# Kernel tuning notes

Measured on AMD Instinct MI355X. Metric: run time of the kernel, lower is better.

## Reference

```python
import jax, jax.numpy as jnp
import numpy as np

D_MODEL = 1024
N_HEADS = 16
N_KV_HEADS = 4
HEAD_DIM = 64   # d_model // total_n_heads
KEY_DIM = 64    # defaults to head_dim
N_REP = N_HEADS // N_KV_HEADS
ATTN_SCALE = 1.0 / np.sqrt(HEAD_DIM)
B, S = 2, 2048


def apply_rope(x, cos, sin):
    # x: [B,S,H,Dh]; cos/sin: [S,Dh//2]; pairs are (x[2j], x[2j+1]) per llama-style apply_rotary_emb
    xr, xi = x[..., ::2], x[..., 1::2]
    c = cos[None, :, None, :]
    s = sin[None, :, None, :]
    out_r = xr * c - xi * s
    out_i = xr * s + xi * c
    return jnp.stack([out_r, out_i], axis=-1).reshape(x.shape)


def setup_inputs() -> dict:
    key = jax.random.key(0)
    ks = jax.random.split(key, 7)
    query = jax.random.normal(ks[0], (B, S, D_MODEL), jnp.float32)
    k_in = jax.random.normal(ks[1], (B, S, D_MODEL), jnp.float32)
    v_in = jax.random.normal(ks[2], (B, S, D_MODEL), jnp.float32)
    # real RoPE frequency tables (theta=10000)
    inv_freq = 1.0 / (10000.0 ** (np.arange(0, KEY_DIM, 2, dtype=np.float32) / KEY_DIM))
    ang = np.outer(np.arange(S, dtype=np.float32), inv_freq)  # [S, KEY_DIM//2]
    freqs_cos = jnp.asarray(np.cos(ang), jnp.float32)
    freqs_sin = jnp.asarray(np.sin(ang), jnp.float32)
    sc = D_MODEL ** -0.5
    wq = jax.random.normal(ks[3], (N_HEADS * KEY_DIM, D_MODEL), jnp.float32) * sc
    wk = jax.random.normal(ks[4], (N_KV_HEADS * KEY_DIM, D_MODEL), jnp.float32) * sc
    wv = jax.random.normal(ks[5], (N_KV_HEADS * HEAD_DIM, D_MODEL), jnp.float32) * sc
    wo = jax.random.normal(ks[6], (N_HEADS * HEAD_DIM, N_HEADS * HEAD_DIM), jnp.float32) * sc
    return {"query": query, "key": k_in, "value": v_in,
            "freqs_cos": freqs_cos, "freqs_sin": freqs_sin,
            "wq": wq, "wk": wk, "wv": wv, "wo": wo}


def reference(query, key, value, freqs_cos, freqs_sin, wq, wk, wv, wo):
    b, sq, _ = query.shape
    sk = key.shape[1]
    xq = (query @ wq.T).reshape(b, sq, N_HEADS, KEY_DIM)
    xk = (key @ wk.T).reshape(b, sk, N_KV_HEADS, KEY_DIM)
    xv = (value @ wv.T).reshape(b, sk, N_KV_HEADS, HEAD_DIM)
    xq = apply_rope(xq, freqs_cos, freqs_sin)
    xk = apply_rope(xk, freqs_cos, freqs_sin)
    # GQA: repeat kv heads (equivalent to torch repeat_kv expand+reshape)
    xk = jnp.repeat(xk, N_REP, axis=2)
    xv = jnp.repeat(xv, N_REP, axis=2)
    scores = jnp.einsum('bqhd,bkhd->bhqk', xq, xk) * ATTN_SCALE
    causal = jnp.tril(jnp.ones((sq, sk), dtype=bool))
    scores = jnp.where(causal[None, None, :, :], scores, -jnp.inf)
    attn = jax.nn.softmax(scores, axis=-1)
    out = jnp.einsum('bhqk,bkhd->bqhd', attn, xv).reshape(b, sq, N_HEADS * HEAD_DIM)
    return out @ wo.T
```

## Files before the change

### kernel.cpp

```cpp
#include <hip/hip_runtime.h>

#define DM 1024
#define NHEADS 16
#define NKVH 4
#define HDIM 64
#define NB 2
#define SEQ 2048
#define MTOK (NB*SEQ)

typedef __attribute__((ext_vector_type(4))) float f32x4;
typedef __attribute__((ext_vector_type(8))) short short8;
typedef unsigned short u16;
typedef unsigned int u32;

__device__ __forceinline__ u16 f2b(float f) {
  u32 i; __builtin_memcpy(&i, &f, 4);
  u32 r = i + 0x7fffu + ((i >> 16) & 1u);
  return (u16)(r >> 16);
}
__device__ __forceinline__ u32 cvtpk(float a, float b) {
  u32 r; asm("v_cvt_pk_bf16_f32 %0, %1, %2" : "=v"(r) : "v"(a), "v"(b)); return r;
}
__device__ __forceinline__ void gload16(const void* g, void* l) {
  __builtin_amdgcn_global_load_lds((const __attribute__((address_space(1))) u32*)g,
                                   (__attribute__((address_space(3))) u32*)l, 16, 0, 0);
}

__device__ __forceinline__ void cvt8(const float* __restrict__ src, u16* __restrict__ dst, int i) {
  float4 a = *(const float4*)(src + i);
  float4 b = *(const float4*)(src + i + 4);
  uint4 pk;
  pk.x = cvtpk(a.x, a.y);
  pk.y = cvtpk(a.z, a.w);
  pk.z = cvtpk(b.x, b.y);
  pk.w = cvtpk(b.z, b.w);
  *(uint4*)(dst + i) = pk;
}

__global__ __launch_bounds__(256) void cvt_all(const float* __restrict__ q, const float* __restrict__ k,
                                               const float* __restrict__ v, const float* __restrict__ wq,
                                               const float* __restrict__ wk, const float* __restrict__ wv,
                                               const float* __restrict__ wo, u16* oq, u16* ok, u16* ov,
                                               u16* owq, u16* owk, u16* owv, u16* owo) {
  const int ACT = (MTOK * DM) / 2048;
  const int BIG = (DM * DM) / 2048;
  const int SML = (256 * DM) / 2048;
  int bid = blockIdx.x;
  const float* s; u16* d;
  if (bid < ACT) { s = q; d = oq; }
  else if (bid < 2 * ACT) { s = k; d = ok; bid -= ACT; }
  else if (bid < 3 * ACT) { s = v; d = ov; bid -= 2 * ACT; }
  else {
    bid -= 3 * ACT;
    if (bid < BIG) { s = wq; d = owq; }
    else if (bid < 2 * BIG) { s = wo; d = owo; bid -= BIG; }
    else if (bid < 2 * BIG + SML) { s = wk; d = owk; bid -= 2 * BIG; }
    else { s = wv; d = owv; bid -= 2 * BIG + SML; }
  }
  cvt8(s, d, (bid * 256 + threadIdx.x) * 8);
}

template<int NR>
__device__ __forceinline__ void stage_tile(const u16* __restrict__ src, int k0, u16* lds,
                                           int w, int lane) {
#pragma unroll
  for (int i = 0; i < NR / 32; i++) {
    const int base = (i * 4 + w) * 1024;
    const int row = (base >> 7) + (lane >> 3);
    const int g = lane & 7;
    gload16(src + (size_t)row * DM + k0 + ((g ^ (row & 7)) << 3), (char*)lds + base);
  }
}
__device__ __forceinline__ short8 lds_frag(const u16* L, int row, int gr) {
  return *(const short8*)(L + row * 64 + ((gr ^ (row & 7)) << 3));
}

__global__ __launch_bounds__(256, 3) void gemm_qkv(const u16* __restrict__ Aq, const u16* __restrict__ Ak,
                                                   const u16* __restrict__ Av, const u16* __restrict__ wq,
                                                   const u16* __restrict__ wk, const u16* __restrict__ wv,
                                                   const float* __restrict__ cosb, const float* __restrict__ sinb,
                                                   u16* __restrict__ Qr, u16* __restrict__ Kr,
                                                   u16* __restrict__ Vt) {
  __shared__ __attribute__((aligned(16))) u16 SH[12288];
  u16* As = SH;
  u16* Bs = SH + 4096;
  const int tid = threadIdx.x, lane = tid & 63, w = tid >> 6;
  const int wr = w >> 1, wc = w & 1, lo = lane & 15, hi = lane >> 4;
  const int bx = blockIdx.x, by = blockIdx.y;
  const int m0 = bx * 64;

  const u16 *Ap, *Wp;
  int n0, mode;
  if (by < 8) { Ap = Aq; Wp = wq; n0 = by * 128; mode = 0; }
  else if (by < 10) { Ap = Ak; Wp = wk; n0 = (by - 8) * 128; mode = 1; }
  else { Ap = Av; Wp = wv; n0 = (by - 10) * 128; mode = 2; }
  const u16* Abase = Ap + (size_t)m0 * DM;
  const u16* Wbase = Wp + (size_t)n0 * DM;

  f32x4 acc[2][4];
#pragma unroll
  for (int i = 0; i < 2; i++)
#pragma unroll
    for (int j = 0; j < 4; j++) acc[i][j] = (f32x4){0.f, 0.f, 0.f, 0.f};

  for (int ks = 0; ks < 16; ks++) {
    const int k0 = ks * 64;
    stage_tile<64>(Abase, k0, As, w, lane);
    stage_tile<128>(Wbase, k0, Bs, w, lane);
    __syncthreads();
    short8 af[2][2], bfr[4][2];
#pragma unroll
    for (int mi = 0; mi < 2; mi++)
#pragma unroll
      for (int kk = 0; kk < 2; kk++)
        af[mi][kk] = lds_frag(As, wr * 32 + mi * 16 + lo, kk * 4 + hi);
#pragma unroll
    for (int ni = 0; ni < 4; ni++)
#pragma unroll
      for (int kk = 0; kk < 2; kk++)
        bfr[ni][kk] = lds_frag(Bs, wc * 64 + ni * 16 + lo, kk * 4 + hi);
    __builtin_amdgcn_s_setprio(1);
#pragma unroll
    for (int mi = 0; mi < 2; mi++)
#pragma unroll
      for (int ni = 0; ni < 4; ni++) {
        acc[mi][ni] = __builtin_amdgcn_mfma_f32_16x16x32_bf16(af[mi][0], bfr[ni][0], acc[mi][ni], 0, 0, 0);
        acc[mi][ni] = __builtin_amdgcn_mfma_f32_16x16x32_bf16(af[mi][1], bfr[ni][1], acc[mi][ni], 0, 0, 0);
      }
    __builtin_amdgcn_s_setprio(0);
    __syncthreads();
  }

  if (mode < 2) {
    const float scale = (mode == 0) ? 0.18033688f : 1.0f;
    u16* outp = (mode == 0) ? Qr : Kr;
    const int OH = (mode == 0) ? NHEADS : NKVH;
    const float sgn = (lo & 1) ? 1.0f : -1.0f;
#pragma unroll
    for (int ni = 0; ni < 4; ni++) {
      const int col = n0 + wc * 64 + ni * 16 + lo;
      const int h = col >> 6, d = col & 63, j = d >> 1;
#pragma unroll
      for (int mi = 0; mi < 2; mi++)
#pragma unroll
        for (int r = 0; r < 4; r++) {
          int row = m0 + wr * 32 + mi * 16 + hi * 4 + r;
          int srow = row & (SEQ - 1), bb = row >> 11;
          float v = acc[mi][ni][r];
          float pv = __shfl_xor(v, 1, 64);
          float c = cosb[srow * 32 + j];
          float s = sinb[srow * 32 + j];
          outp[((size_t)(bb * OH + h) * SEQ + srow) * 64 + d] = f2b((v * c + pv * s * sgn) * scale);
        }
    }
  } else {
    u16* Tt = SH;
#pragma unroll
    for (int mi = 0; mi < 2; mi++)
#pragma unroll
      for (int ni = 0; ni < 4; ni++) {
        const int cl = wc * 64 + ni * 16 + lo;
#pragma unroll
        for (int r = 0; r < 4; r++) {
          int rl = wr * 32 + mi * 16 + hi * 4 + r;
          Tt[cl * 72 + rl] = f2b(acc[mi][ni][r]);
        }
      }
    __syncthreads();
    const int dl = tid >> 1;
    const int sh2 = (tid & 1) * 32;
    const int dg = n0 + dl;
    const int kh = dg >> 6, drow = dg & 63;
    const int bb = m0 >> 11, sbase = m0 & (SEQ - 1);
    u16* dst = Vt + ((size_t)(bb * NKVH + kh) * 64 + drow) * SEQ + sbase + sh2;
#pragma unroll
    for (int i = 0; i < 4; i++)
      *(uint4*)(dst + i * 8) = *(const uint4*)&Tt[dl * 72 + sh2 + i * 8];
  }
}

__device__ __forceinline__ void softmax_pv(f32x4 (&sc)[4], float& m, float& lsp, f32x4 (&o)[4],
                                           const short8* vb0, const short8* vb1, int hi) {
  float lm = sc[0][0];
#pragma unroll
  for (int f = 0; f < 4; f++)
#pragma unroll
    for (int r = 0; r < 4; r++) lm = fmaxf(lm, sc[f][r]);
  if (__any(lm - m > 8.f)) {
    float mx = fmaxf(m, lm);
    mx = fmaxf(mx, __shfl_xor(mx, 16, 64));
    mx = fmaxf(mx, __shfl_xor(mx, 32, 64));
    float corr = exp2f(m - mx);
    m = mx;
    lsp *= corr;
    float corrq[4];
#pragma unroll
    for (int r = 0; r < 4; r++) corrq[r] = __shfl(corr, hi * 4 + r, 64);
#pragma unroll
    for (int nf = 0; nf < 4; nf++)
#pragma unroll
      for (int r = 0; r < 4; r++) o[nf][r] *= corrq[r];
  }
  float pv2[4][4];
#pragma unroll
  for (int f = 0; f < 4; f++)
#pragma unroll
    for (int r = 0; r < 4; r++) {
      pv2[f][r] = exp2f(sc[f][r] - m);
      lsp += pv2[f][r];
    }
  union { u32 u[4]; short8 s8; } pa0, pa1;
#pragma unroll
  for (int t = 0; t < 4; t++) {
    int fsel = t >> 1, r0 = 2 * (t & 1);
    pa0.u[t] = cvtpk(pv2[fsel][r0], pv2[fsel][r0 + 1]);
    pa1.u[t] = cvtpk(pv2[2 + fsel][r0], pv2[2 + fsel][r0 + 1]);
  }
  __builtin_amdgcn_s_setprio(1);
#pragma unroll
  for (int nf = 0; nf < 4; nf++) {
    o[nf] = __builtin_amdgcn_mfma_f32_16x16x32_bf16(pa0.s8, vb0[nf], o[nf], 0, 0, 0);
    o[nf] = __builtin_amdgcn_mfma_f32_16x16x32_bf16(pa1.s8, vb1[nf], o[nf], 0, 0, 0);
  }
  __builtin_amdgcn_s_setprio(0);
}

__global__ __launch_bounds__(256, 2) void attn_kernel(const u16* __restrict__ Q, const u16* __restrict__ Kb,
                                                      const u16* __restrict__ Vt, u16* __restrict__ AO) {
  __shared__ __attribute__((aligned(16))) u16 Ks[2][4096];
  __shared__ __attribute__((aligned(16))) u16 Vs[2][4096];
  const int tid = threadIdx.x;
  const int w = tid >> 6, lane = tid & 63;
  const int lo = lane & 15, hi = lane >> 4;
  const int bh = blockIdx.x;
  const int b = bh >> 4, h = bh & 15, kh = h >> 2;
  const int yy = blockIdx.y;
  const int p = (yy < 8) ? yy : 23 - yy;
  const int tA = p, tB = 31 - p;
  const int q0A = tA * 64 + w * 16;
  const int q0B = tB * 64 + w * 16;
  const u16* Qp = Q + (size_t)bh * SEQ * 64;
  const u16* Kp = Kb + (size_t)(b * NKVH + kh) * SEQ * 64;
  const u16* Vp = Vt + (size_t)(b * NKVH + kh) * 64 * SEQ;

  short8 qfA[2], qfB[2];
#pragma unroll
  for (int kk = 0; kk < 2; kk++) {
    qfA[kk] = *(const short8*)(Qp + (size_t)(q0A + lo) * 64 + kk * 32 + hi * 8);
    qfB[kk] = *(const short8*)(Qp + (size_t)(q0B + lo) * 64 + kk * 32 + hi * 8);
  }

  f32x4 oA[4], oB[4];
#pragma unroll
  for (int nf = 0; nf < 4; nf++) { oA[nf] = (f32x4){0.f,0.f,0.f,0.f}; oB[nf] = (f32x4){0.f,0.f,0.f,0.f}; }
  float mA = -__builtin_inff(), lspA = 0.f;
  float mB = -__builtin_inff(), lspB = 0.f;

  auto key = [](int row) { return (row & 3) | (((row >> 3) & 1) << 2); };
  auto stage = [&](int kv0, int bufi) {
#pragma unroll
    for (int s = 0; s < 2; s++) {
      int base = s * 4096 + w * 1024;
      int o2 = base + (lane << 4);
      int row = o2 >> 7;
      int gg = ((o2 >> 4) & 7) ^ key(row);
      gload16(Kp + (size_t)(kv0 + row) * 64 + gg * 8, (char*)&Ks[bufi][0] + base);
      gload16(Vp + (size_t)row * SEQ + kv0 + gg * 8, (char*)&Vs[bufi][0] + base);
    }
  };
  auto lds8 = [&](const u16* S, int row, int col8) {
    return *(const short8*)(S + row * 64 + (col8 ^ (key(row) << 3)));
  };

  int krow[4];
#pragma unroll
  for (int f = 0; f < 4; f++)
    krow[f] = 32 * (f >> 1) + 8 * (lo >> 2) + 4 * (f & 1) + (lo & 3);

  const int nt = tB + 1;
  stage(0, 0);
  __syncthreads();

  for (int c = 0; c < nt; ++c) {
    const int cur = c & 1;
    const int kv0 = c * 64;
    if (c + 1 < nt) stage(kv0 + 64, cur ^ 1);

    short8 kf0[4], kf1[4];
#pragma unroll
    for (int f = 0; f < 4; f++) {
      kf0[f] = lds8(&Ks[cur][0], krow[f], hi * 8);
      kf1[f] = lds8(&Ks[cur][0], krow[f], 32 + hi * 8);
    }
    const bool actA = (c <= tA);

    f32x4 scB[4], scA[4];
#pragma unroll
    for (int f = 0; f < 4; f++) scB[f] = (f32x4){0.f,0.f,0.f,0.f};
    __builtin_amdgcn_s_setprio(1);
#pragma unroll
    for (int f = 0; f < 4; f++) {
      scB[f] = __builtin_amdgcn_mfma_f32_16x16x32_bf16(kf0[f], qfB[0], scB[f], 0, 0, 0);
      scB[f] = __builtin_amdgcn_mfma_f32_16x16x32_bf16(kf1[f], qfB[1], scB[f], 0, 0, 0);
    }
    __builtin_amdgcn_s_setprio(0);
    if (actA) {
#pragma unroll
      for (int f = 0; f < 4; f++) scA[f] = (f32x4){0.f,0.f,0.f,0.f};
      __builtin_amdgcn_s_setprio(1);
#pragma unroll
      for (int f = 0; f < 4; f++) {
        scA[f] = __builtin_amdgcn_mfma_f32_16x16x32_bf16(kf0[f], qfA[0], scA[f], 0, 0, 0);
        scA[f] = __builtin_amdgcn_mfma_f32_16x16x32_bf16(kf1[f], qfA[1], scA[f], 0, 0, 0);
      }
      __builtin_amdgcn_s_setprio(0);
    }

    short8 vb0[4], vb1[4];
#pragma unroll
    for (int nf = 0; nf < 4; nf++) {
      vb0[nf] = lds8(&Vs[cur][0], nf * 16 + lo, hi * 8);
      vb1[nf] = lds8(&Vs[cur][0], nf * 16 + lo, 32 + hi * 8);
    }

    if (c == tB) {
#pragma unroll
      for (int f = 0; f < 4; f++) {
        int kvb = kv0 + 32 * (f >> 1) + 8 * hi + 4 * (f & 1);
#pragma unroll
        for (int r = 0; r < 4; r++)
          if (kvb + r > q0B + lo) scB[f][r] = -__builtin_inff();
      }
    }
    softmax_pv(scB, mB, lspB, oB, vb0, vb1, hi);

    if (actA) {
      if (c == tA) {
#pragma unroll
        for (int f = 0; f < 4; f++) {
          int kvb = kv0 + 32 * (f >> 1) + 8 * hi + 4 * (f & 1);
#pragma unroll
          for (int r = 0; r < 4; r++)
            if (kvb + r > q0A + lo) scA[f][r] = -__builtin_inff();
        }
      }
      softmax_pv(scA, mA, lspA, oA, vb0, vb1, hi);
    }
    __syncthreads();
  }

#pragma unroll
  for (int t2 = 0; t2 < 2; t2++) {
    float lsp = t2 ? lspB : lspA;
    const int q0 = t2 ? q0B : q0A;
    f32x4* o = t2 ? oB : oA;
    lsp += __shfl_xor(lsp, 16, 64);
    lsp += __shfl_xor(lsp, 32, 64);
    float inv = 1.0f / lsp;
    float invq[4];
#pragma unroll
    for (int r = 0; r < 4; r++) invq[r] = __shfl(inv, hi * 4 + r, 64);
#pragma unroll
    for (int nf = 0; nf < 4; nf++)
#pragma unroll
      for (int r = 0; r < 4; r++) {
        int q = q0 + hi * 4 + r;
        int d = nf * 16 + lo;
        AO[((size_t)(b * SEQ + q) * NHEADS + h) * 64 + d] = f2b(o[nf][r] * invq[r]);
      }
  }
}

__global__ __launch_bounds__(256, 2) void gemm_out(const u16* __restrict__ A, const u16* __restrict__ W,
                                                   float* __restrict__ Out) {
  __shared__ __attribute__((aligned(16))) u16 SH[12288];
  u16* As = SH;
  u16* Bs = SH + 4096;
  const int tid = threadIdx.x, lane = tid & 63, w = tid >> 6;
  const int wr = w >> 1, wc = w & 1, lo = lane & 15, hi = lane >> 4;
  const int m0 = blockIdx.x * 64, n0 = blockIdx.y * 128;
  const u16* Abase = A + (size_t)m0 * DM;
  const u16* Wbase = W + (size_t)n0 * DM;

  f32x4 acc[2][4];
#pragma unroll
  for (int i = 0; i < 2; i++)
#pragma unroll
    for (int j = 0; j < 4; j++) acc[i][j] = (f32x4){0.f, 0.f, 0.f, 0.f};

  for (int ks = 0; ks < 16; ks++) {
    const int k0 = ks * 64;
    stage_tile<64>(Abase, k0, As, w, lane);
    stage_tile<128>(Wbase, k0, Bs, w, lane);
    __syncthreads();
    short8 af[2][2], bfr[4][2];
#pragma unroll
    for (int mi = 0; mi < 2; mi++)
#pragma unroll
      for (int kk = 0; kk < 2; kk++)
        af[mi][kk] = lds_frag(As, wr * 32 + mi * 16 + lo, kk * 4 + hi);
#pragma unroll
    for (int ni = 0; ni < 4; ni++)
#pragma unroll
      for (int kk = 0; kk < 2; kk++)
        bfr[ni][kk] = lds_frag(Bs, wc * 64 + ni * 16 + lo, kk * 4 + hi);
    __builtin_amdgcn_s_setprio(1);
#pragma unroll
    for (int mi = 0; mi < 2; mi++)
#pragma unroll
      for (int ni = 0; ni < 4; ni++) {
        acc[mi][ni] = __builtin_amdgcn_mfma_f32_16x16x32_bf16(af[mi][0], bfr[ni][0], acc[mi][ni], 0, 0, 0);
        acc[mi][ni] = __builtin_amdgcn_mfma_f32_16x16x32_bf16(af[mi][1], bfr[ni][1], acc[mi][ni], 0, 0, 0);
      }
    __builtin_amdgcn_s_setprio(0);
    __syncthreads();
  }

#pragma unroll
  for (int mi = 0; mi < 2; mi++)
#pragma unroll
    for (int ni = 0; ni < 4; ni++)
#pragma unroll
      for (int r = 0; r < 4; r++) {
        int row = m0 + wr * 32 + mi * 16 + hi * 4 + r;
        int col = n0 + wc * 64 + ni * 16 + lo;
        Out[(size_t)row * DM + col] = acc[mi][ni][r];
      }
}

extern "C" void kernel_launch(void* const* d_in, const int* in_sizes, int n_in,
                              void* d_out, int out_size, void* d_ws, size_t ws_size,
                              hipStream_t stream) {
  const float* query = (const float*)d_in[0];
  const float* key_ = (const float*)d_in[1];
  const float* value = (const float*)d_in[2];
  const float* fcos = (const float*)d_in[3];
  const float* fsin = (const float*)d_in[4];
  const float* wq = (const float*)d_in[5];
  const float* wk = (const float*)d_in[6];
  const float* wv = (const float*)d_in[7];
  const float* wo = (const float*)d_in[8];

  char* ws = (char*)d_ws;
  size_t off = 0;
  auto alloc = [&](size_t elems) {
    u16* p = (u16*)(ws + off);
    off = (off + elems * 2 + 255) & ~(size_t)255;
    return p;
  };
  u16* qf = alloc((size_t)MTOK * DM);
  u16* kf = alloc((size_t)MTOK * DM);
  u16* vf = alloc((size_t)MTOK * DM);
  u16* wqf = alloc((size_t)DM * DM);
  u16* wkf = alloc((size_t)256 * DM);
  u16* wvf = alloc((size_t)256 * DM);
  u16* wof = alloc((size_t)DM * DM);
  u16* Qr = alloc((size_t)MTOK * DM);
  u16* Kr = alloc((size_t)NB * NKVH * SEQ * 64);
  u16* Vt = alloc((size_t)NB * NKVH * 64 * SEQ);
  u16* AO = alloc((size_t)MTOK * DM);

  cvt_all<<<3 * 2048 + 1280, 256, 0, stream>>>(query, key_, value, wq, wk, wv, wo,
                                               qf, kf, vf, wqf, wkf, wvf, wof);

  gemm_qkv<<<dim3(64, 12), 256, 0, stream>>>(qf, kf, vf, wqf, wkf, wvf,
                                             fcos, fsin, Qr, Kr, Vt);

  attn_kernel<<<dim3(NB * NHEADS, 16), 256, 0, stream>>>(Qr, Kr, Vt, AO);

  gemm_out<<<dim3(64, 8), 256, 0, stream>>>(AO, wof, (float*)d_out);
}
```

Before: 93.50 us.

## Serialize paired causal tiles into a uniform 33-unit loop with triple-buffered LDS

Restructures the attention loop so each block processes its short tile A's KV chunks first and then tile B's, giving exactly 33 units per block. K/V staging moves from double to triple buffering with explicit vmcnt waits and a single barrier per unit, prefetching two units ahead. It also drops the remapped blockIdx.y ordering. K/V chunks shared between tiles A and B are now loaded twice, and LDS use grows by half, which may cut occupancy.

After: 97.18 us. 1.04x slower.

```diff
diff --git a/kernel.cpp b/kernel.cpp
--- a/kernel.cpp
+++ b/kernel.cpp
@@ -227,15 +227,14 @@
 
 __global__ __launch_bounds__(256, 2) void attn_kernel(const u16* __restrict__ Q, const u16* __restrict__ Kb,
                                                       const u16* __restrict__ Vt, u16* __restrict__ AO) {
-  __shared__ __attribute__((aligned(16))) u16 Ks[2][4096];
-  __shared__ __attribute__((aligned(16))) u16 Vs[2][4096];
+  __shared__ __attribute__((aligned(16))) u16 Ks[3][4096];
+  __shared__ __attribute__((aligned(16))) u16 Vs[3][4096];
   const int tid = threadIdx.x;
   const int w = tid >> 6, lane = tid & 63;
   const int lo = lane & 15, hi = lane >> 4;
   const int bh = blockIdx.x;
   const int b = bh >> 4, h = bh & 15, kh = h >> 2;
-  const int yy = blockIdx.y;
-  const int p = (yy < 8) ? yy : 23 - yy;
+  const int p = blockIdx.y;
   const int tA = p, tB = 31 - p;
   const int q0A = tA * 64 + w * 16;
   const int q0B = tB * 64 + w * 16;
@@ -277,76 +276,62 @@
   for (int f = 0; f < 4; f++)
     krow[f] = 32 * (f >> 1) + 8 * (lo >> 2) + 4 * (f & 1) + (lo & 3);
 
-  const int nt = tB + 1;
-  stage(0, 0);
-  __syncthreads();
-
-  for (int c = 0; c < nt; ++c) {
-    const int cur = c & 1;
-    const int kv0 = c * 64;
-    if (c + 1 < nt) stage(kv0 + 64, cur ^ 1);
-
+  auto do_unit = [&](const u16* Kcur, const u16* Vcur, short8 (&qf)[2], float& m, float& lsp,
+                     f32x4 (&o)[4], int q0, bool straddle, int kv0) {
     short8 kf0[4], kf1[4];
 #pragma unroll
     for (int f = 0; f < 4; f++) {
-      kf0[f] = lds8(&Ks[cur][0], krow[f], hi * 8);
-      kf1[f] = lds8(&Ks[cur][0], krow[f], 32 + hi * 8);
-    }
-    const bool actA = (c <= tA);
-
-    f32x4 scB[4], scA[4];
-#pragma unroll
-    for (int f = 0; f < 4; f++) scB[f] = (f32x4){0.f,0.f,0.f,0.f};
+      kf0[f] = lds8(Kcur, krow[f], hi * 8);
+      kf1[f] = lds8(Kcur, krow[f], 32 + hi * 8);
+    }
+    f32x4 sc[4];
+#pragma unroll
+    for (int f = 0; f < 4; f++) sc[f] = (f32x4){0.f, 0.f, 0.f, 0.f};
     __builtin_amdgcn_s_setprio(1);
 #pragma unroll
     for (int f = 0; f < 4; f++) {
-      scB[f] = __builtin_amdgcn_mfma_f32_16x16x32_bf16(kf0[f], qfB[0], scB[f], 0, 0, 0);
-      scB[f] = __builtin_amdgcn_mfma_f32_16x16x32_bf16(kf1[f], qfB[1], scB[f], 0, 0, 0);
+      sc[f] = __builtin_amdgcn_mfma_f32_16x16x32_bf16(kf0[f], qf[0], sc[f], 0, 0, 0);
+      sc[f] = __builtin_amdgcn_mfma_f32_16x16x32_bf16(kf1[f], qf[1], sc[f], 0, 0, 0);
     }
     __builtin_amdgcn_s_setprio(0);
-    if (actA) {
-#pragma unroll
-      for (int f = 0; f < 4; f++) scA[f] = (f32x4){0.f,0.f,0.f,0.f};
-      __builtin_amdgcn_s_setprio(1);
-#pragma unroll
-      for (int f = 0; f < 4; f++) {
-        scA[f] = __builtin_amdgcn_mfma_f32_16x16x32_bf16(kf0[f], qfA[0], scA[f], 0, 0, 0);
-        scA[f] = __builtin_amdgcn_mfma_f32_16x16x32_bf16(kf1[f], qfA[1], scA[f], 0, 0, 0);
-      }
-      __builtin_amdgcn_s_setprio(0);
-    }
-
     short8 vb0[4], vb1[4];
 #pragma unroll
     for (int nf = 0; nf < 4; nf++) {
-      vb0[nf] = lds8(&Vs[cur][0], nf * 16 + lo, hi * 8);
-      vb1[nf] = lds8(&Vs[cur][0], nf * 16 + lo, 32 + hi * 8);
-    }
-
-    if (c == tB) {
+      vb0[nf] = lds8(Vcur, nf * 16 + lo, hi * 8);
+      vb1[nf] = lds8(Vcur, nf * 16 + lo, 32 + hi * 8);
+    }
+    if (straddle) {
 #pragma unroll
       for (int f = 0; f < 4; f++) {
         int kvb = kv0 + 32 * (f >> 1) + 8 * hi + 4 * (f & 1);
 #pragma unroll
         for (int r = 0; r < 4; r++)
-          if (kvb + r > q0B + lo) scB[f][r] = -__builtin_inff();
-      }
-    }
-    softmax_pv(scB, mB, lspB, oB, vb0, vb1, hi);
-
-    if (actA) {
-      if (c == tA) {
-#pragma unroll
-        for (int f = 0; f < 4; f++) {
-          int kvb = kv0 + 32 * (f >> 1) + 8 * hi + 4 * (f & 1);
-#pragma unroll
-          for (int r = 0; r < 4; r++)
-            if (kvb + r > q0A + lo) scA[f][r] = -__builtin_inff();
-        }
-      }
-      softmax_pv(scA, mA, lspA, oA, vb0, vb1, hi);
-    }
-    __syncthreads();
+          if (kvb + r > q0 + lo) sc[f][r] = -__builtin_inff();
+      }
+    }
+    softmax_pv(sc, m, lsp, o, vb0, vb1, hi);
+  };
+
+  stage(0, 0);
+  stage(((1 <= p) ? 1 : 0) * 64, 1);
+  int b0 = 0;
+  for (int u = 0; u < 33; ++u) {
+    if (u < 32) asm volatile("s_waitcnt vmcnt(4)" ::: "memory");
+    else        asm volatile("s_waitcnt vmcnt(0)" ::: "memory");
+    __builtin_amdgcn_s_barrier();
+    int bs = b0 + 2; if (bs >= 3) bs -= 3;
+    if (u + 2 < 33) {
+      int un = u + 2;
+      int kvn = (un <= p) ? un : (un - p - 1);
+      stage(kvn * 64, bs);
+    }
+    const int kvci = (u <= p) ? u : (u - p - 1);
+    const int kv0 = kvci * 64;
+    const u16* Kcur = &Ks[b0][0];
+    const u16* Vcur = &Vs[b0][0];
+    if (u <= p) do_unit(Kcur, Vcur, qfA, mA, lspA, oA, q0A, u == p, kv0);
+    else        do_unit(Kcur, Vcur, qfB, mB, lspB, oB, q0B, u == 32, kv0);
+    b0++; if (b0 == 3) b0 = 0;
   }
 
 #pragma unroll
```

## Split paired causal q-tiles into one tile per block with longest-first order

Applied to the files above, without the earlier changes.

The attention kernel stops pairing a short and a long causal query tile in each block, which had shared the K/V loads between them. Each block now handles a single 64-row query tile, the grid doubles along y, and blocks are issued longest tile first. Launch bounds are raised to 4 blocks per SM to give more occupancy. In exchange each K/V tile is staged from global memory more often, since the sharing between paired tiles is lost, and register use per thread must fit the tighter limit.

Result: no change. 94.38 us (+0.9%).

```diff
diff --git a/kernel.cpp b/kernel.cpp
--- a/kernel.cpp
+++ b/kernel.cpp
@@ -225,7 +225,7 @@
   __builtin_amdgcn_s_setprio(0);
 }
 
-__global__ __launch_bounds__(256, 2) void attn_kernel(const u16* __restrict__ Q, const u16* __restrict__ Kb,
+__global__ __launch_bounds__(256, 4) void attn_kernel(const u16* __restrict__ Q, const u16* __restrict__ Kb,
                                                       const u16* __restrict__ Vt, u16* __restrict__ AO) {
   __shared__ __attribute__((aligned(16))) u16 Ks[2][4096];
   __shared__ __attribute__((aligned(16))) u16 Vs[2][4096];
@@ -234,27 +234,21 @@
   const int lo = lane & 15, hi = lane >> 4;
   const int bh = blockIdx.x;
   const int b = bh >> 4, h = bh & 15, kh = h >> 2;
-  const int yy = blockIdx.y;
-  const int p = (yy < 8) ? yy : 23 - yy;
-  const int tA = p, tB = 31 - p;
-  const int q0A = tA * 64 + w * 16;
-  const int q0B = tB * 64 + w * 16;
+  const int t = 31 - blockIdx.y;
+  const int q0 = t * 64 + w * 16;
   const u16* Qp = Q + (size_t)bh * SEQ * 64;
   const u16* Kp = Kb + (size_t)(b * NKVH + kh) * SEQ * 64;
   const u16* Vp = Vt + (size_t)(b * NKVH + kh) * 64 * SEQ;
 
-  short8 qfA[2], qfB[2];
-#pragma unroll
-  for (int kk = 0; kk < 2; kk++) {
-    qfA[kk] = *(const short8*)(Qp + (size_t)(q0A + lo) * 64 + kk * 32 + hi * 8);
-    qfB[kk] = *(const short8*)(Qp + (size_t)(q0B + lo) * 64 + kk * 32 + hi * 8);
-  }
-
-  f32x4 oA[4], oB[4];
-#pragma unroll
-  for (int nf = 0; nf < 4; nf++) { oA[nf] = (f32x4){0.f,0.f,0.f,0.f}; oB[nf] = (f32x4){0.f,0.f,0.f,0.f}; }
-  float mA = -__builtin_inff(), lspA = 0.f;
-  float mB = -__builtin_inff(), lspB = 0.f;
+  short8 qf[2];
+#pragma unroll
+  for (int kk = 0; kk < 2; kk++)
+    qf[kk] = *(const short8*)(Qp + (size_t)(q0 + lo) * 64 + kk * 32 + hi * 8);
+
+  f32x4 o[4];
+#pragma unroll
+  for (int nf = 0; nf < 4; nf++) o[nf] = (f32x4){0.f, 0.f, 0.f, 0.f};
+  float m = -__builtin_inff(), lsp = 0.f;
 
   auto key = [](int row) { return (row & 3) | (((row >> 3) & 1) << 2); };
   auto stage = [&](int kv0, int bufi) {
@@ -277,7 +271,7 @@
   for (int f = 0; f < 4; f++)
     krow[f] = 32 * (f >> 1) + 8 * (lo >> 2) + 4 * (f & 1) + (lo & 3);
 
-  const int nt = tB + 1;
+  const int nt = t + 1;
   stage(0, 0);
   __syncthreads();
 
@@ -292,29 +286,16 @@
       kf0[f] = lds8(&Ks[cur][0], krow[f], hi * 8);
       kf1[f] = lds8(&Ks[cur][0], krow[f], 32 + hi * 8);
     }
-    const bool actA = (c <= tA);
-
-    f32x4 scB[4], scA[4];
-#pragma unroll
-    for (int f = 0; f < 4; f++) scB[f] = (f32x4){0.f,0.f,0.f,0.f};
+    f32x4 sc[4];
+#pragma unroll
+    for (int f = 0; f < 4; f++) sc[f] = (f32x4){0.f, 0.f, 0.f, 0.f};
     __builtin_amdgcn_s_setprio(1);
 #pragma unroll
     for (int f = 0; f < 4; f++) {
-      scB[f] = __builtin_amdgcn_mfma_f32_16x16x32_bf16(kf0[f], qfB[0], scB[f], 0, 0, 0);
-      scB[f] = __builtin_amdgcn_mfma_f32_16x16x32_bf16(kf1[f], qfB[1], scB[f], 0, 0, 0);
+      sc[f] = __builtin_amdgcn_mfma_f32_16x16x32_bf16(kf0[f], qf[0], sc[f], 0, 0, 0);
+      sc[f] = __builtin_amdgcn_mfma_f32_16x16x32_bf16(kf1[f], qf[1], sc[f], 0, 0, 0);
     }
     __builtin_amdgcn_s_setprio(0);
-    if (actA) {
-#pragma unroll
-      for (int f = 0; f < 4; f++) scA[f] = (f32x4){0.f,0.f,0.f,0.f};
-      __builtin_amdgcn_s_setprio(1);
-#pragma unroll
-      for (int f = 0; f < 4; f++) {
-        scA[f] = __builtin_amdgcn_mfma_f32_16x16x32_bf16(kf0[f], qfA[0], scA[f], 0, 0, 0);
-        scA[f] = __builtin_amdgcn_mfma_f32_16x16x32_bf16(kf1[f], qfA[1], scA[f], 0, 0, 0);
-      }
-      __builtin_amdgcn_s_setprio(0);
-    }
 
     short8 vb0[4], vb1[4];
 #pragma unroll
@@ -323,52 +304,33 @@
       vb1[nf] = lds8(&Vs[cur][0], nf * 16 + lo, 32 + hi * 8);
     }
 
-    if (c == tB) {
+    if (c == t) {
 #pragma unroll
       for (int f = 0; f < 4; f++) {
         int kvb = kv0 + 32 * (f >> 1) + 8 * hi + 4 * (f & 1);
 #pragma unroll
         for (int r = 0; r < 4; r++)
-          if (kvb + r > q0B + lo) scB[f][r] = -__builtin_inff();
+          if (kvb + r > q0 + lo) sc[f][r] = -__builtin_inff();
       }
     }
-    softmax_pv(scB, mB, lspB, oB, vb0, vb1, hi);
-
-    if (actA) {
-      if (c == tA) {
-#pragma unroll
-        for (int f = 0; f < 4; f++) {
-          int kvb = kv0 + 32 * (f >> 1) + 8 * hi + 4 * (f & 1);
-#pragma unroll
-          for (int r = 0; r < 4; r++)
-            if (kvb + r > q0A + lo) scA[f][r] = -__builtin_inff();
-        }
-      }
-      softmax_pv(scA, mA, lspA, oA, vb0, vb1, hi);
-    }
-    __syncthreads();
-  }
-
-#pragma unroll
-  for (int t2 = 0; t2 < 2; t2++) {
-    float lsp = t2 ? lspB : lspA;
-    const int q0 = t2 ? q0B : q0A;
-    f32x4* o = t2 ? oB : oA;
-    lsp += __shfl_xor(lsp, 16, 64);
-    lsp += __shfl_xor(lsp, 32, 64);
-    float inv = 1.0f / lsp;
-    float invq[4];
-#pragma unroll
-    for (int r = 0; r < 4; r++) invq[r] = __shfl(inv, hi * 4 + r, 64);
-#pragma unroll
-    for (int nf = 0; nf < 4; nf++)
-#pragma unroll
-      for (int r = 0; r < 4; r++) {
-        int q = q0 + hi * 4 + r;
-        int d = nf * 16 + lo;
-        AO[((size_t)(b * SEQ + q) * NHEADS + h) * 64 + d] = f2b(o[nf][r] * invq[r]);
-      }
-  }
+    softmax_pv(sc, m, lsp, o, vb0, vb1, hi);
+    __syncthreads();
+  }
+
+  lsp += __shfl_xor(lsp, 16, 64);
+  lsp += __shfl_xor(lsp, 32, 64);
+  float inv = 1.0f / lsp;
+  float invq[4];
+#pragma unroll
+  for (int r = 0; r < 4; r++) invq[r] = __shfl(inv, hi * 4 + r, 64);
+#pragma unroll
+  for (int nf = 0; nf < 4; nf++)
+#pragma unroll
+    for (int r = 0; r < 4; r++) {
+      int q = q0 + hi * 4 + r;
+      int d = nf * 16 + lo;
+      AO[((size_t)(b * SEQ + q) * NHEADS + h) * 64 + d] = f2b(o[nf][r] * invq[r]);
+    }
 }
 
 __global__ __launch_bounds__(256, 2) void gemm_out(const u16* __restrict__ A, const u16* __restrict__ W,
@@ -466,7 +428,7 @@
   gemm_qkv<<<dim3(64, 12), 256, 0, stream>>>(qf, kf, vf, wqf, wkf, wvf,
                                              fcos, fsin, Qr, Kr, Vt);
 
-  attn_kernel<<<dim3(NB * NHEADS, 16), 256, 0, stream>>>(Qr, Kr, Vt, AO);
+  attn_kernel<<<dim3(NB * NHEADS, 32), 256, 0, stream>>>(Qr, Kr, Vt, AO);
 
   gemm_out<<<dim3(64, 8), 256, 0, stream>>>(AO, wof, (float*)d_out);
 }
```
